# Performance work log

Hardware: AMD Instinct MI355X
Metric: run time of the kernel (lower is better)

The kernel has to match this reference:

```python
import jax, jax.numpy as jnp
import numpy as np

D_MODEL = 1024
NUM_HEADS = 16
D_LATENT = 256
HEAD_DIM = D_MODEL // NUM_HEADS
BATCH = 2048
SEQ = 32


def setup_inputs() -> dict:
    key = jax.random.key(0)
    ks = jax.random.split(key, 9)
    s = 1.0 / np.sqrt(D_MODEL)
    sl = 1.0 / np.sqrt(D_LATENT)
    return {
        "x": jax.random.normal(ks[0], (BATCH, SEQ, D_MODEL), dtype=jnp.float32),
        "memory": jax.random.normal(ks[1], (BATCH, SEQ, D_LATENT), dtype=jnp.float32),
        "W_q": jax.random.normal(ks[2], (D_MODEL, D_MODEL), dtype=jnp.float32) * s,
        "W_k": jax.random.normal(ks[3], (D_MODEL, D_MODEL), dtype=jnp.float32) * s,
        "W_v": jax.random.normal(ks[4], (D_MODEL, D_MODEL), dtype=jnp.float32) * s,
        "W_o": jax.random.normal(ks[5], (D_MODEL, D_MODEL), dtype=jnp.float32) * s,
        "W_down_kv": jax.random.normal(ks[6], (D_MODEL, D_LATENT), dtype=jnp.float32) * s,
        "W_up_k": jax.random.normal(ks[7], (D_LATENT, D_MODEL), dtype=jnp.float32) * sl,
        "W_up_v": jax.random.normal(ks[8], (D_LATENT, D_MODEL), dtype=jnp.float32) * sl,
    }


def reference(x, memory, W_q, W_k, W_v, W_o, W_down_kv, W_up_k, W_up_v):
    B, S, _ = x.shape
    q = x @ W_q                     # [B,S,D]
    k = x @ W_k
    v = x @ W_v
    latent_kv = (k + v) @ W_down_kv  # [B,S,L]
    latent_kv = jnp.nan_to_num((latent_kv + memory) * 0.5)
    k_rec = latent_kv @ W_up_k       # [B,S,D]
    v_rec = latent_kv @ W_up_v
    # split heads: [B,H,S,hd]
    qh = q.reshape(B, S, NUM_HEADS, HEAD_DIM).transpose(0, 2, 1, 3)
    kh = k_rec.reshape(B, S, NUM_HEADS, HEAD_DIM).transpose(0, 2, 1, 3)
    vh = v_rec.reshape(B, S, NUM_HEADS, HEAD_DIM).transpose(0, 2, 1, 3)
    # NOTE: faithful to source — scale is sqrt(d_model), not sqrt(head_dim)
    scores = jnp.einsum("bhqd,bhkd->bhqk", qh, kh) / jnp.sqrt(jnp.float32(D_MODEL))
    scores = jnp.nan_to_num(scores, nan=0.0, posinf=10.0, neginf=-10.0)
    attn = jax.nn.softmax(scores, axis=-1)
    ctx = jnp.einsum("bhqk,bhkd->bhqd", attn, vh)
    ctx = ctx.transpose(0, 2, 1, 3).reshape(B, S, D_MODEL)
    out = ctx @ W_o
    return out, latent_kv
```

## Files before the change

kernel.cpp:

```cpp
#include <hip/hip_runtime.h>
#include <hip/hip_bf16.h>

typedef unsigned short u16;
typedef __attribute__((ext_vector_type(8))) __bf16 bf16x8;
typedef __attribute__((ext_vector_type(8))) unsigned short u16x8;
typedef __attribute__((ext_vector_type(4))) float floatx4;
typedef __attribute__((ext_vector_type(16))) float floatx16;

#define AS1 __attribute__((address_space(1)))
#define AS3 __attribute__((address_space(3)))

__device__ __forceinline__ u16 f2bf(float f) {
  unsigned u = __float_as_uint(f);
  u += 0x7fffu + ((u >> 16) & 1u);
  return (u16)(u >> 16);
}

__device__ __forceinline__ void g2lds16(const u16* g, u16* l) {
  __builtin_amdgcn_global_load_lds((AS1 void*)g, (AS3 void*)l, 16, 0, 0);
}

__global__ __launch_bounds__(256) void k_cvt_bf16(const float* __restrict__ s,
                                                  u16* __restrict__ d, long n) {
  long i = ((long)blockIdx.x * blockDim.x + threadIdx.x) * 8;
  long stride = (long)gridDim.x * blockDim.x * 8;
  for (; i < n; i += stride) {
    float4 a = *(const float4*)(s + i);
    float4 b = *(const float4*)(s + i + 4);
    u16x8 o;
    o[0] = f2bf(a.x); o[1] = f2bf(a.y); o[2] = f2bf(a.z); o[3] = f2bf(a.w);
    o[4] = f2bf(b.x); o[5] = f2bf(b.y); o[6] = f2bf(b.z); o[7] = f2bf(b.w);
    *(u16x8*)(d + i) = o;
  }
}

__global__ __launch_bounds__(256) void k_addcvt(const float* __restrict__ s0,
                                                const float* __restrict__ s1,
                                                u16* __restrict__ d, long n) {
  long i = ((long)blockIdx.x * blockDim.x + threadIdx.x) * 8;
  long stride = (long)gridDim.x * blockDim.x * 8;
  for (; i < n; i += stride) {
    float4 a0 = *(const float4*)(s0 + i);
    float4 a1 = *(const float4*)(s0 + i + 4);
    float4 b0 = *(const float4*)(s1 + i);
    float4 b1 = *(const float4*)(s1 + i + 4);
    u16x8 o;
    o[0] = f2bf(a0.x + b0.x); o[1] = f2bf(a0.y + b0.y);
    o[2] = f2bf(a0.z + b0.z); o[3] = f2bf(a0.w + b0.w);
    o[4] = f2bf(a1.x + b1.x); o[5] = f2bf(a1.y + b1.y);
    o[6] = f2bf(a1.z + b1.z); o[7] = f2bf(a1.w + b1.w);
    *(u16x8*)(d + i) = o;
  }
}

__global__ __launch_bounds__(256) void k_tcvt(const float* __restrict__ s,
                                              u16* __restrict__ d, int R, int C) {
  __shared__ float t[32][33];
  const int lx = threadIdx.x, ly = threadIdx.y;
  const int bx = blockIdx.x * 32;
  const int by = blockIdx.y * 32;
  #pragma unroll
  for (int i = 0; i < 32; i += 8)
    t[ly + i][lx] = s[(size_t)(by + ly + i) * C + bx + lx];
  __syncthreads();
  #pragma unroll
  for (int i = 0; i < 32; i += 8)
    d[(size_t)(bx + ly + i) * R + by + lx] = f2bf(t[lx][ly + i]);
}


#define MFMA16(a, b, c) c = __builtin_amdgcn_mfma_f32_16x16x32_bf16(a, b, c, 0, 0, 0)

template <int MODE>
__global__ __launch_bounds__(256, 3) void gemm128(
    const u16* __restrict__ A, const u16* __restrict__ Bt,
    int M, int N, int K, int ntn,
    u16* __restrict__ Cb, float* __restrict__ Cf,
    const float* __restrict__ memp, float* __restrict__ latf, u16* __restrict__ latb) {
  __shared__ u16 As[128 * 64];
  __shared__ u16 Bs[128 * 64];
  const int tid = threadIdx.x;
  const int lane = tid & 63;
  const int wid = tid >> 6;
  const int wr = wid >> 1, wc = wid & 1;

  int bid = blockIdx.x;
  {
    const int nwg = gridDim.x;
    const int q = nwg >> 3, r = nwg & 7;
    const int xcd = bid & 7, idx = bid >> 3;
    bid = (xcd < r ? xcd * (q + 1) : r * (q + 1) + (xcd - r) * q) + idx;
  }
  const int mt = bid / ntn, nt = bid % ntn;
  const int m0 = mt * 128, n0 = nt * 128;

  const int fr = lane & 15;
  const int g8 = (lane >> 4) * 8;
  const int xr = (lane & 7) * 8;

  floatx4 acc[4][4];
  #pragma unroll
  for (int i = 0; i < 4; i++)
    #pragma unroll
    for (int j = 0; j < 4; j++) acc[i][j] = 0.0f;

  const u16* Ag0 = A + (size_t)m0 * K;
  const u16* Bg0 = Bt + (size_t)n0 * K;

  for (int kt = 0; kt < K; kt += 64) {
    #pragma unroll
    for (int p = 0; p < 4; p++) {
      int ci = p * 256 + tid;
      int row = ci >> 3;
      int kc = ((ci & 7) ^ (row & 7)) * 8;
      g2lds16(Ag0 + (size_t)row * K + kt + kc, &As[ci * 8]);
    }
    #pragma unroll
    for (int p = 0; p < 4; p++) {
      int ci = p * 256 + tid;
      int row = ci >> 3;
      int kc = ((ci & 7) ^ (row & 7)) * 8;
      g2lds16(Bg0 + (size_t)row * K + kt + kc, &Bs[ci * 8]);
    }
    __syncthreads();
    #pragma unroll
    for (int kk = 0; kk < 64; kk += 32) {
      const int koff = kk + g8;
      bf16x8 af[4], bfv[4];
      #pragma unroll
      for (int i = 0; i < 4; i++)
        af[i] = *(const bf16x8*)&As[(wr * 64 + i * 16 + fr) * 64 + (koff ^ xr)];
      #pragma unroll
      for (int j = 0; j < 4; j++)
        bfv[j] = *(const bf16x8*)&Bs[(wc * 64 + j * 16 + fr) * 64 + (koff ^ xr)];
      #pragma unroll
      for (int i = 0; i < 4; i++)
        #pragma unroll
        for (int j = 0; j < 4; j++)
          MFMA16(af[i], bfv[j], acc[i][j]);
    }
    __syncthreads();
  }

  #pragma unroll
  for (int i = 0; i < 4; i++) {
    const int mb = m0 + wr * 64 + i * 16 + ((lane >> 4) * 4);
    #pragma unroll
    for (int j = 0; j < 4; j++) {
      const int cb = n0 + wc * 64 + j * 16 + (lane & 15);
      #pragma unroll
      for (int r = 0; r < 4; r++) {
        const int m = mb + r;
        const float v = acc[i][j][r];
        if (MODE == 0) {
          Cb[(size_t)m * N + cb] = f2bf(v);
        } else if (MODE == 1) {
          if (n0 < 1024) {
            Cb[(size_t)m * 1024 + cb] = f2bf(v);
          } else {
            int lc = cb - 1024;
            float lv = (v + memp[(size_t)m * 256 + lc]) * 0.5f;
            latf[(size_t)m * 256 + lc] = lv;
            latb[(size_t)m * 256 + lc] = f2bf(lv);
          }
        } else {
          Cf[(size_t)m * N + cb] = v;
        }
      }
    }
  }
}

__global__ __launch_bounds__(256) void k_attn(const u16* __restrict__ KV, u16* Q) {
  __shared__ u16 Qs[4][32][72];
  __shared__ u16 Ks[4][32][72];
  __shared__ u16 Vt[4][64][40];
  const int tid = threadIdx.x;
  const int hg = blockIdx.x;
  const int b = blockIdx.y;
  const long tok0 = (long)b * 32;

  {
    const int t = tid >> 3, ci = tid & 7;
    const int hd = ci >> 1, c0 = (ci & 1) * 32;
    const u16* qrow = Q + (tok0 + t) * 1024 + hg * 256 + ci * 32;
    #pragma unroll
    for (int u = 0; u < 4; u++)
      *(u16x8*)&Qs[hd][t][c0 + u * 8] = *(const u16x8*)(qrow + u * 8);
    const u16* krow = KV + (tok0 + t) * 2048 + hg * 256 + ci * 32;
    #pragma unroll
    for (int u = 0; u < 4; u++)
      *(u16x8*)&Ks[hd][t][c0 + u * 8] = *(const u16x8*)(krow + u * 8);
    const u16* vrow = KV + (tok0 + t) * 2048 + 1024 + hg * 256 + ci * 32;
    #pragma unroll
    for (int u = 0; u < 4; u++) {
      u16x8 v = *(const u16x8*)(vrow + u * 8);
      #pragma unroll
      for (int j = 0; j < 8; j++) Vt[hd][c0 + u * 8 + j][t] = v[j];
    }
  }
  __syncthreads();

  const int w = tid >> 6;
  const int lane = tid & 63;
  const int col = lane & 31, hi = lane >> 5;

  floatx16 S;
  #pragma unroll
  for (int r = 0; r < 16; r++) S[r] = 0.0f;
  #pragma unroll
  for (int kc = 0; kc < 4; kc++) {
    bf16x8 aq = *(const bf16x8*)&Qs[w][col][kc * 16 + hi * 8];
    bf16x8 bk = *(const bf16x8*)&Ks[w][col][kc * 16 + hi * 8];
    S = __builtin_amdgcn_mfma_f32_32x32x16_bf16(aq, bk, S, 0, 0, 0);
  }

  u16* Pw = &Qs[w][0][0];
  float pr[16];
  #pragma unroll
  for (int r = 0; r < 16; r++) {
    float sc = S[r] * 0.03125f;
    float mx = sc;
    #pragma unroll
    for (int off = 16; off >= 1; off >>= 1) mx = fmaxf(mx, __shfl_xor(mx, off, 64));
    float e = __expf(sc - mx);
    float sm = e;
    #pragma unroll
    for (int off = 16; off >= 1; off >>= 1) sm += __shfl_xor(sm, off, 64);
    pr[r] = e / sm;
  }
  #pragma unroll
  for (int r = 0; r < 16; r++) {
    int row = (r & 3) + 8 * (r >> 2) + 4 * hi;
    Pw[row * 40 + col] = f2bf(pr[r]);
  }
  __syncthreads();

  floatx16 c0v, c1v;
  #pragma unroll
  for (int r = 0; r < 16; r++) { c0v[r] = 0.0f; c1v[r] = 0.0f; }
  #pragma unroll
  for (int kc = 0; kc < 2; kc++) {
    bf16x8 ap = *(const bf16x8*)&Pw[col * 40 + kc * 16 + hi * 8];
    bf16x8 bv0 = *(const bf16x8*)&Vt[w][col][kc * 16 + hi * 8];
    bf16x8 bv1 = *(const bf16x8*)&Vt[w][32 + col][kc * 16 + hi * 8];
    c0v = __builtin_amdgcn_mfma_f32_32x32x16_bf16(ap, bv0, c0v, 0, 0, 0);
    c1v = __builtin_amdgcn_mfma_f32_32x32x16_bf16(ap, bv1, c1v, 0, 0, 0);
  }
  #pragma unroll
  for (int r = 0; r < 16; r++) {
    int row = (r & 3) + 8 * (r >> 2) + 4 * hi;
    u16* orow = Q + (tok0 + row) * 1024 + hg * 256 + w * 64;
    orow[col] = f2bf(c0v[r]);
    orow[col + 32] = f2bf(c1v[r]);
  }
}

extern "C" void kernel_launch(void* const* d_in, const int* in_sizes, int n_in,
                              void* d_out, int out_size, void* d_ws, size_t ws_size,
                              hipStream_t stream) {
  const float* x    = (const float*)d_in[0];
  const float* mem  = (const float*)d_in[1];
  const float* W_q  = (const float*)d_in[2];
  const float* W_k  = (const float*)d_in[3];
  const float* W_v  = (const float*)d_in[4];
  const float* W_o  = (const float*)d_in[5];
  const float* W_dn = (const float*)d_in[6];
  const float* W_uk = (const float*)d_in[7];
  const float* W_uv = (const float*)d_in[8];
  float* out  = (float*)d_out;
  float* latf = out + (size_t)67108864;

  char* wp = (char*)d_ws;
  u16* Qb  = (u16*)wp; wp += (size_t)65536 * 1024 * 2;
  u16* Lb  = (u16*)wp; wp += (size_t)65536 * 256 * 2;
  u16* WAt = (u16*)wp; wp += (size_t)1280 * 1024 * 2;
  u16* WBt = (u16*)wp; wp += (size_t)2048 * 256 * 2;
  u16* Wot = (u16*)wp; wp += (size_t)1024 * 1024 * 2;
  u16* Wdt = (u16*)wp; wp += (size_t)256 * 1024 * 2;
  u16* Wkv = (u16*)wp; wp += (size_t)1024 * 1024 * 2;

  u16* Xb  = (u16*)d_out;
  u16* KVb = (u16*)d_out;

  dim3 b256(256);
  dim3 tb(32, 8);
  k_cvt_bf16<<<4096, b256, 0, stream>>>(x, Xb, (long)67108864);
  k_addcvt<<<512, b256, 0, stream>>>(W_k, W_v, Wkv, (long)1048576);
  k_tcvt<<<dim3(32, 32), tb, 0, stream>>>(W_q, WAt, 1024, 1024);
  k_tcvt<<<dim3(8, 32),  tb, 0, stream>>>(W_dn, Wdt, 1024, 256);
  k_tcvt<<<dim3(32, 8),  tb, 0, stream>>>(W_uk, WBt, 256, 1024);
  k_tcvt<<<dim3(32, 8),  tb, 0, stream>>>(W_uv, WBt + (size_t)1024 * 256, 256, 1024);
  k_tcvt<<<dim3(32, 32), tb, 0, stream>>>(W_o, Wot, 1024, 1024);

  gemm128<0><<<16, b256, 0, stream>>>(
      Wdt, Wkv, 256, 1024, 1024, 8, WAt + (size_t)1024 * 1024,
      nullptr, nullptr, nullptr, nullptr);

  gemm128<1><<<5120, b256, 0, stream>>>(
      Xb, WAt, 65536, 1280, 1024, 10, Qb, nullptr, mem, latf, Lb);

  gemm128<0><<<8192, b256, 0, stream>>>(
      Lb, WBt, 65536, 2048, 256, 16, KVb, nullptr, nullptr, nullptr, nullptr);

  k_attn<<<dim3(4, 2048), b256, 0, stream>>>(KVb, Qb);

  gemm128<2><<<4096, b256, 0, stream>>>(
      Qb, Wot, 65536, 1024, 1024, 8, nullptr, out, nullptr, nullptr, nullptr);
}
```

Before: 798.5 us.

## Fuse latent up-projection into attention via absorbed K/V weights

```diff
diff --git a/kernel.cpp b/kernel.cpp
--- a/kernel.cpp
+++ b/kernel.cpp
@@ -2,6 +2,7 @@
 #include <hip/hip_bf16.h>
 
 typedef unsigned short u16;
+typedef unsigned int u32;
 typedef __attribute__((ext_vector_type(8))) __bf16 bf16x8;
 typedef __attribute__((ext_vector_type(8))) unsigned short u16x8;
 typedef __attribute__((ext_vector_type(4))) float floatx4;
@@ -68,8 +69,8 @@
     d[(size_t)(bx + ly + i) * R + by + lx] = f2bf(t[lx][ly + i]);
 }
 
-
 #define MFMA16(a, b, c) c = __builtin_amdgcn_mfma_f32_16x16x32_bf16(a, b, c, 0, 0, 0)
+#define MFMA32(a, b, c) c = __builtin_amdgcn_mfma_f32_32x32x16_bf16(a, b, c, 0, 0, 0)
 
 template <int MODE>
 __global__ __launch_bounds__(256, 3) void gemm128(
@@ -171,88 +172,132 @@
   }
 }
 
-__global__ __launch_bounds__(256) void k_attn(const u16* __restrict__ KV, u16* Q) {
-  __shared__ u16 Qs[4][32][72];
-  __shared__ u16 Ks[4][32][72];
-  __shared__ u16 Vt[4][64][40];
+__device__ __forceinline__ void pack_lds(u16* T, const floatx16& d,
+                                         int col, int hi, bf16x8& f0, bf16x8& f1) {
+  #pragma unroll
+  for (int i = 0; i < 8; i++) {
+    const int r = 2 * i;
+    const int rr = (r & 3) + 8 * (r >> 2) + 4 * hi;
+    const u32 wv = (u32)f2bf(d[r]) | ((u32)f2bf(d[r + 1]) << 16);
+    *(u32*)&T[col * 40 + rr] = wv;
+  }
+  f0 = *(const bf16x8*)&T[col * 40 + hi * 8];
+  f1 = *(const bf16x8*)&T[col * 40 + 16 + hi * 8];
+}
+
+__global__ __launch_bounds__(256, 3) void k_attn2(
+    const u16* __restrict__ Lb,
+    u16* __restrict__ Q,
+    const u16* __restrict__ Wuk,
+    const u16* __restrict__ WuvT)
+{
+  __shared__ u16 Ls[32][264];
+  __shared__ u16 LsT[256][40];
+  __shared__ u16 Tw[4][32][40];
   const int tid = threadIdx.x;
-  const int hg = blockIdx.x;
-  const int b = blockIdx.y;
-  const long tok0 = (long)b * 32;
+  const long tok0 = (long)blockIdx.x * 32;
 
   {
-    const int t = tid >> 3, ci = tid & 7;
-    const int hd = ci >> 1, c0 = (ci & 1) * 32;
-    const u16* qrow = Q + (tok0 + t) * 1024 + hg * 256 + ci * 32;
-    #pragma unroll
-    for (int u = 0; u < 4; u++)
-      *(u16x8*)&Qs[hd][t][c0 + u * 8] = *(const u16x8*)(qrow + u * 8);
-    const u16* krow = KV + (tok0 + t) * 2048 + hg * 256 + ci * 32;
-    #pragma unroll
-    for (int u = 0; u < 4; u++)
-      *(u16x8*)&Ks[hd][t][c0 + u * 8] = *(const u16x8*)(krow + u * 8);
-    const u16* vrow = KV + (tok0 + t) * 2048 + 1024 + hg * 256 + ci * 32;
+    const int key = tid >> 3, c0 = (tid & 7) * 32;
     #pragma unroll
     for (int u = 0; u < 4; u++) {
-      u16x8 v = *(const u16x8*)(vrow + u * 8);
-      #pragma unroll
-      for (int j = 0; j < 8; j++) Vt[hd][c0 + u * 8 + j][t] = v[j];
+      u16x8 v = *(const u16x8*)(Lb + (tok0 + key) * 256 + c0 + u * 8);
+      *(u16x8*)&Ls[key][c0 + u * 8] = v;
+      #pragma unroll
+      for (int j = 0; j < 8; j++) LsT[c0 + u * 8 + j][key] = v[j];
     }
   }
   __syncthreads();
 
   const int w = tid >> 6;
   const int lane = tid & 63;
-  const int col = lane & 31, hi = lane >> 5;
-
-  floatx16 S;
-  #pragma unroll
-  for (int r = 0; r < 16; r++) S[r] = 0.0f;
-  #pragma unroll
-  for (int kc = 0; kc < 4; kc++) {
-    bf16x8 aq = *(const bf16x8*)&Qs[w][col][kc * 16 + hi * 8];
-    bf16x8 bk = *(const bf16x8*)&Ks[w][col][kc * 16 + hi * 8];
-    S = __builtin_amdgcn_mfma_f32_32x32x16_bf16(aq, bk, S, 0, 0, 0);
-  }
-
-  u16* Pw = &Qs[w][0][0];
-  float pr[16];
-  #pragma unroll
-  for (int r = 0; r < 16; r++) {
-    float sc = S[r] * 0.03125f;
-    float mx = sc;
-    #pragma unroll
-    for (int off = 16; off >= 1; off >>= 1) mx = fmaxf(mx, __shfl_xor(mx, off, 64));
-    float e = __expf(sc - mx);
-    float sm = e;
-    #pragma unroll
-    for (int off = 16; off >= 1; off >>= 1) sm += __shfl_xor(sm, off, 64);
-    pr[r] = e / sm;
-  }
-  #pragma unroll
-  for (int r = 0; r < 16; r++) {
-    int row = (r & 3) + 8 * (r >> 2) + 4 * hi;
-    Pw[row * 40 + col] = f2bf(pr[r]);
-  }
-  __syncthreads();
-
-  floatx16 c0v, c1v;
-  #pragma unroll
-  for (int r = 0; r < 16; r++) { c0v[r] = 0.0f; c1v[r] = 0.0f; }
-  #pragma unroll
-  for (int kc = 0; kc < 2; kc++) {
-    bf16x8 ap = *(const bf16x8*)&Pw[col * 40 + kc * 16 + hi * 8];
-    bf16x8 bv0 = *(const bf16x8*)&Vt[w][col][kc * 16 + hi * 8];
-    bf16x8 bv1 = *(const bf16x8*)&Vt[w][32 + col][kc * 16 + hi * 8];
-    c0v = __builtin_amdgcn_mfma_f32_32x32x16_bf16(ap, bv0, c0v, 0, 0, 0);
-    c1v = __builtin_amdgcn_mfma_f32_32x32x16_bf16(ap, bv1, c1v, 0, 0, 0);
-  }
-  #pragma unroll
-  for (int r = 0; r < 16; r++) {
-    int row = (r & 3) + 8 * (r >> 2) + 4 * hi;
-    u16* orow = Q + (tok0 + row) * 1024 + hg * 256 + w * 64;
-    orow[col] = f2bf(c0v[r]);
-    orow[col + 32] = f2bf(c1v[r]);
+  const int col = lane & 31;
+  const int hi = lane >> 5;
+  const int hi8 = hi * 8;
+  const int rhi4 = hi * 4;
+  u16* T = &Tw[w][0][0];
+
+  #pragma unroll 1
+  for (int hh = 0; hh < 4; hh++) {
+    const int h = w + hh * 4;
+
+    const u16* qbase = Q + (tok0 + col) * 1024 + h * 64 + hi8;
+    bf16x8 qf[4];
+    #pragma unroll
+    for (int ks = 0; ks < 4; ks++)
+      qf[ks] = *(const bf16x8*)(qbase + ks * 16);
+
+    floatx16 St;
+    #pragma unroll
+    for (int r = 0; r < 16; r++) St[r] = 0.0f;
+    #pragma unroll
+    for (int mi = 0; mi < 8; mi++) {
+      floatx16 qt;
+      #pragma unroll
+      for (int r = 0; r < 16; r++) qt[r] = 0.0f;
+      #pragma unroll
+      for (int ks = 0; ks < 4; ks++) {
+        bf16x8 af = *(const bf16x8*)(Wuk + (size_t)(mi * 32 + col) * 1024 +
+                                     h * 64 + ks * 16 + hi8);
+        MFMA32(af, qf[ks], qt);
+      }
+      bf16x8 qg0, qg1;
+      pack_lds(T, qt, col, hi, qg0, qg1);
+      bf16x8 la0 = *(const bf16x8*)&Ls[col][mi * 32 + hi8];
+      MFMA32(la0, qg0, St);
+      bf16x8 la1 = *(const bf16x8*)&Ls[col][mi * 32 + 16 + hi8];
+      MFMA32(la1, qg1, St);
+    }
+
+    float p[16];
+    float mx = -3.4e38f;
+    #pragma unroll
+    for (int r = 0; r < 16; r++) { p[r] = St[r] * 0.03125f; mx = fmaxf(mx, p[r]); }
+    mx = fmaxf(mx, __shfl_xor(mx, 32, 64));
+    float sm = 0.0f;
+    #pragma unroll
+    for (int r = 0; r < 16; r++) { p[r] = __expf(p[r] - mx); sm += p[r]; }
+    sm += __shfl_xor(sm, 32, 64);
+    const float rs = 1.0f / sm;
+    floatx16 Pt;
+    #pragma unroll
+    for (int r = 0; r < 16; r++) Pt[r] = p[r] * rs;
+    bf16x8 pg0, pg1;
+    pack_lds(T, Pt, col, hi, pg0, pg1);
+
+    floatx16 cacc0, cacc1;
+    #pragma unroll
+    for (int r = 0; r < 16; r++) { cacc0[r] = 0.0f; cacc1[r] = 0.0f; }
+    const u16* wv0 = WuvT + (size_t)(h * 64 + col) * 256;
+    const u16* wv1 = WuvT + (size_t)(h * 64 + 32 + col) * 256;
+    #pragma unroll
+    for (int mi = 0; mi < 8; mi++) {
+      floatx16 ct;
+      #pragma unroll
+      for (int r = 0; r < 16; r++) ct[r] = 0.0f;
+      bf16x8 lt0 = *(const bf16x8*)&LsT[mi * 32 + col][hi8];
+      MFMA32(lt0, pg0, ct);
+      bf16x8 lt1 = *(const bf16x8*)&LsT[mi * 32 + col][16 + hi8];
+      MFMA32(lt1, pg1, ct);
+      bf16x8 cg0, cg1;
+      pack_lds(T, ct, col, hi, cg0, cg1);
+      #pragma unroll
+      for (int ksl = 0; ksl < 2; ksl++) {
+        bf16x8 cg = ksl ? cg1 : cg0;
+        bf16x8 b0 = *(const bf16x8*)(wv0 + mi * 32 + ksl * 16 + hi8);
+        bf16x8 b1 = *(const bf16x8*)(wv1 + mi * 32 + ksl * 16 + hi8);
+        MFMA32(cg, b0, cacc0);
+        MFMA32(cg, b1, cacc1);
+      }
+    }
+
+    #pragma unroll
+    for (int r = 0; r < 16; r++) {
+      const int rr = (r & 3) + 8 * (r >> 2) + rhi4;
+      u16* orow = Q + (tok0 + rr) * 1024 + h * 64;
+      orow[col] = f2bf(cacc0[r]);
+      orow[32 + col] = f2bf(cacc1[r]);
+    }
   }
 }
 
@@ -272,25 +317,25 @@
   float* latf = out + (size_t)67108864;
 
   char* wp = (char*)d_ws;
-  u16* Qb  = (u16*)wp; wp += (size_t)65536 * 1024 * 2;
-  u16* Lb  = (u16*)wp; wp += (size_t)65536 * 256 * 2;
-  u16* WAt = (u16*)wp; wp += (size_t)1280 * 1024 * 2;
-  u16* WBt = (u16*)wp; wp += (size_t)2048 * 256 * 2;
-  u16* Wot = (u16*)wp; wp += (size_t)1024 * 1024 * 2;
-  u16* Wdt = (u16*)wp; wp += (size_t)256 * 1024 * 2;
-  u16* Wkv = (u16*)wp; wp += (size_t)1024 * 1024 * 2;
-
-  u16* Xb  = (u16*)d_out;
-  u16* KVb = (u16*)d_out;
+  u16* Qb   = (u16*)wp; wp += (size_t)65536 * 1024 * 2;
+  u16* Lb   = (u16*)wp; wp += (size_t)65536 * 256 * 2;
+  u16* WAt  = (u16*)wp; wp += (size_t)1280 * 1024 * 2;
+  u16* WuvT = (u16*)wp; wp += (size_t)1024 * 256 * 2;
+  u16* Wot  = (u16*)wp; wp += (size_t)1024 * 1024 * 2;
+  u16* Wdt  = (u16*)wp; wp += (size_t)256 * 1024 * 2;
+  u16* Wkv  = (u16*)wp; wp += (size_t)1024 * 1024 * 2;
+  u16* Wukb = (u16*)wp; wp += (size_t)256 * 1024 * 2;
+
+  u16* Xb = (u16*)d_out;
 
   dim3 b256(256);
   dim3 tb(32, 8);
   k_cvt_bf16<<<4096, b256, 0, stream>>>(x, Xb, (long)67108864);
   k_addcvt<<<512, b256, 0, stream>>>(W_k, W_v, Wkv, (long)1048576);
+  k_cvt_bf16<<<128, b256, 0, stream>>>(W_uk, Wukb, (long)262144);
   k_tcvt<<<dim3(32, 32), tb, 0, stream>>>(W_q, WAt, 1024, 1024);
   k_tcvt<<<dim3(8, 32),  tb, 0, stream>>>(W_dn, Wdt, 1024, 256);
-  k_tcvt<<<dim3(32, 8),  tb, 0, stream>>>(W_uk, WBt, 256, 1024);
-  k_tcvt<<<dim3(32, 8),  tb, 0, stream>>>(W_uv, WBt + (size_t)1024 * 256, 256, 1024);
+  k_tcvt<<<dim3(32, 8),  tb, 0, stream>>>(W_uv, WuvT, 256, 1024);
   k_tcvt<<<dim3(32, 32), tb, 0, stream>>>(W_o, Wot, 1024, 1024);
 
   gemm128<0><<<16, b256, 0, stream>>>(
@@ -300,10 +345,7 @@
   gemm128<1><<<5120, b256, 0, stream>>>(
       Xb, WAt, 65536, 1280, 1024, 10, Qb, nullptr, mem, latf, Lb);
 
-  gemm128<0><<<8192, b256, 0, stream>>>(
-      Lb, WBt, 65536, 2048, 256, 16, KVb, nullptr, nullptr, nullptr, nullptr);
-
-  k_attn<<<dim3(4, 2048), b256, 0, stream>>>(KVb, Qb);
+  k_attn2<<<2048, b256, 0, stream>>>(Lb, Qb, Wukb, WuvT);
 
   gemm128<2><<<4096, b256, 0, stream>>>(
       Qb, Wot, 65536, 1024, 1024, 8, nullptr, out, nullptr, nullptr, nullptr);
```

After: 898.1 us. 12.5% more time.

## Merge prep kernels into one launch and enlarge GEMM tiles to 256x128

Applied to the files above, without the earlier changes.

```diff
diff --git a/kernel.cpp b/kernel.cpp
--- a/kernel.cpp
+++ b/kernel.cpp
@@ -2,6 +2,7 @@
 #include <hip/hip_bf16.h>
 
 typedef unsigned short u16;
+typedef unsigned int u32;
 typedef __attribute__((ext_vector_type(8))) __bf16 bf16x8;
 typedef __attribute__((ext_vector_type(8))) unsigned short u16x8;
 typedef __attribute__((ext_vector_type(4))) float floatx4;
@@ -20,64 +21,82 @@
   __builtin_amdgcn_global_load_lds((AS1 void*)g, (AS3 void*)l, 16, 0, 0);
 }
 
-__global__ __launch_bounds__(256) void k_cvt_bf16(const float* __restrict__ s,
-                                                  u16* __restrict__ d, long n) {
-  long i = ((long)blockIdx.x * blockDim.x + threadIdx.x) * 8;
-  long stride = (long)gridDim.x * blockDim.x * 8;
-  for (; i < n; i += stride) {
-    float4 a = *(const float4*)(s + i);
-    float4 b = *(const float4*)(s + i + 4);
-    u16x8 o;
-    o[0] = f2bf(a.x); o[1] = f2bf(a.y); o[2] = f2bf(a.z); o[3] = f2bf(a.w);
-    o[4] = f2bf(b.x); o[5] = f2bf(b.y); o[6] = f2bf(b.z); o[7] = f2bf(b.w);
-    *(u16x8*)(d + i) = o;
-  }
-}
-
-__global__ __launch_bounds__(256) void k_addcvt(const float* __restrict__ s0,
-                                                const float* __restrict__ s1,
-                                                u16* __restrict__ d, long n) {
-  long i = ((long)blockIdx.x * blockDim.x + threadIdx.x) * 8;
-  long stride = (long)gridDim.x * blockDim.x * 8;
-  for (; i < n; i += stride) {
-    float4 a0 = *(const float4*)(s0 + i);
-    float4 a1 = *(const float4*)(s0 + i + 4);
-    float4 b0 = *(const float4*)(s1 + i);
-    float4 b1 = *(const float4*)(s1 + i + 4);
+__device__ __forceinline__ void tcvt_body(const float* __restrict__ s,
+                                          u16* __restrict__ d, int R, int C,
+                                          int bx, int by, int tid,
+                                          float (*t)[33]) {
+  const int lx = tid & 31, ly = tid >> 5;
+  const int x0 = bx * 32, y0 = by * 32;
+  #pragma unroll
+  for (int i = 0; i < 32; i += 8)
+    t[ly + i][lx] = s[(size_t)(y0 + ly + i) * C + x0 + lx];
+  __syncthreads();
+  #pragma unroll
+  for (int i = 0; i < 32; i += 8)
+    d[(size_t)(x0 + ly + i) * R + y0 + lx] = f2bf(t[lx][ly + i]);
+}
+
+__global__ __launch_bounds__(256) void k_prep(
+    const float* __restrict__ x, u16* __restrict__ Xb,
+    const float* __restrict__ Wk, const float* __restrict__ Wv, u16* __restrict__ Wkv,
+    const float* __restrict__ Wq, u16* __restrict__ WAt,
+    const float* __restrict__ Wdn, u16* __restrict__ Wdt,
+    const float* __restrict__ Wuk, u16* __restrict__ WBt,
+    const float* __restrict__ Wuv, u16* __restrict__ WBt2,
+    const float* __restrict__ Wo, u16* __restrict__ Wot) {
+  __shared__ float t[32][33];
+  const int b = blockIdx.x;
+  const int tid = threadIdx.x;
+  if (b < 4096) {
+    long i = ((long)b * 256 + tid) * 8;
+    const long stride = (long)4096 * 256 * 8;
+    for (; i < 67108864L; i += stride) {
+      float4 a = *(const float4*)(x + i);
+      float4 c = *(const float4*)(x + i + 4);
+      u16x8 o;
+      o[0] = f2bf(a.x); o[1] = f2bf(a.y); o[2] = f2bf(a.z); o[3] = f2bf(a.w);
+      o[4] = f2bf(c.x); o[5] = f2bf(c.y); o[6] = f2bf(c.z); o[7] = f2bf(c.w);
+      *(u16x8*)(Xb + i) = o;
+    }
+  } else if (b < 4608) {
+    long i = ((long)(b - 4096) * 256 + tid) * 8;
+    float4 a0 = *(const float4*)(Wk + i);
+    float4 a1 = *(const float4*)(Wk + i + 4);
+    float4 b0 = *(const float4*)(Wv + i);
+    float4 b1 = *(const float4*)(Wv + i + 4);
     u16x8 o;
     o[0] = f2bf(a0.x + b0.x); o[1] = f2bf(a0.y + b0.y);
     o[2] = f2bf(a0.z + b0.z); o[3] = f2bf(a0.w + b0.w);
     o[4] = f2bf(a1.x + b1.x); o[5] = f2bf(a1.y + b1.y);
     o[6] = f2bf(a1.z + b1.z); o[7] = f2bf(a1.w + b1.w);
-    *(u16x8*)(d + i) = o;
-  }
-}
-
-__global__ __launch_bounds__(256) void k_tcvt(const float* __restrict__ s,
-                                              u16* __restrict__ d, int R, int C) {
-  __shared__ float t[32][33];
-  const int lx = threadIdx.x, ly = threadIdx.y;
-  const int bx = blockIdx.x * 32;
-  const int by = blockIdx.y * 32;
-  #pragma unroll
-  for (int i = 0; i < 32; i += 8)
-    t[ly + i][lx] = s[(size_t)(by + ly + i) * C + bx + lx];
-  __syncthreads();
-  #pragma unroll
-  for (int i = 0; i < 32; i += 8)
-    d[(size_t)(bx + ly + i) * R + by + lx] = f2bf(t[lx][ly + i]);
-}
-
+    *(u16x8*)(Wkv + i) = o;
+  } else if (b < 5632) {
+    int lb = b - 4608;
+    tcvt_body(Wq, WAt, 1024, 1024, lb & 31, lb >> 5, tid, t);
+  } else if (b < 5888) {
+    int lb = b - 5632;
+    tcvt_body(Wdn, Wdt, 1024, 256, lb & 7, lb >> 3, tid, t);
+  } else if (b < 6144) {
+    int lb = b - 5888;
+    tcvt_body(Wuk, WBt, 256, 1024, lb & 31, lb >> 5, tid, t);
+  } else if (b < 6400) {
+    int lb = b - 6144;
+    tcvt_body(Wuv, WBt2, 256, 1024, lb & 31, lb >> 5, tid, t);
+  } else {
+    int lb = b - 6400;
+    tcvt_body(Wo, Wot, 1024, 1024, lb & 31, lb >> 5, tid, t);
+  }
+}
 
 #define MFMA16(a, b, c) c = __builtin_amdgcn_mfma_f32_16x16x32_bf16(a, b, c, 0, 0, 0)
 
 template <int MODE>
-__global__ __launch_bounds__(256, 3) void gemm128(
+__global__ __launch_bounds__(512, 4) void gemm_mn(
     const u16* __restrict__ A, const u16* __restrict__ Bt,
     int M, int N, int K, int ntn,
     u16* __restrict__ Cb, float* __restrict__ Cf,
     const float* __restrict__ memp, float* __restrict__ latf, u16* __restrict__ latb) {
-  __shared__ u16 As[128 * 64];
+  __shared__ u16 As[256 * 64];
   __shared__ u16 Bs[128 * 64];
   const int tid = threadIdx.x;
   const int lane = tid & 63;
@@ -92,7 +111,7 @@
     bid = (xcd < r ? xcd * (q + 1) : r * (q + 1) + (xcd - r) * q) + idx;
   }
   const int mt = bid / ntn, nt = bid % ntn;
-  const int m0 = mt * 128, n0 = nt * 128;
+  const int m0 = mt * 256, n0 = nt * 128;
 
   const int fr = lane & 15;
   const int g8 = (lane >> 4) * 8;
@@ -110,14 +129,14 @@
   for (int kt = 0; kt < K; kt += 64) {
     #pragma unroll
     for (int p = 0; p < 4; p++) {
-      int ci = p * 256 + tid;
+      int ci = p * 512 + tid;
       int row = ci >> 3;
       int kc = ((ci & 7) ^ (row & 7)) * 8;
       g2lds16(Ag0 + (size_t)row * K + kt + kc, &As[ci * 8]);
     }
     #pragma unroll
-    for (int p = 0; p < 4; p++) {
-      int ci = p * 256 + tid;
+    for (int p = 0; p < 2; p++) {
+      int ci = p * 512 + tid;
       int row = ci >> 3;
       int kc = ((ci & 7) ^ (row & 7)) * 8;
       g2lds16(Bg0 + (size_t)row * K + kt + kc, &Bs[ci * 8]);
@@ -284,27 +303,24 @@
   u16* KVb = (u16*)d_out;
 
   dim3 b256(256);
-  dim3 tb(32, 8);
-  k_cvt_bf16<<<4096, b256, 0, stream>>>(x, Xb, (long)67108864);
-  k_addcvt<<<512, b256, 0, stream>>>(W_k, W_v, Wkv, (long)1048576);
-  k_tcvt<<<dim3(32, 32), tb, 0, stream>>>(W_q, WAt, 1024, 1024);
-  k_tcvt<<<dim3(8, 32),  tb, 0, stream>>>(W_dn, Wdt, 1024, 256);
-  k_tcvt<<<dim3(32, 8),  tb, 0, stream>>>(W_uk, WBt, 256, 1024);
-  k_tcvt<<<dim3(32, 8),  tb, 0, stream>>>(W_uv, WBt + (size_t)1024 * 256, 256, 1024);
-  k_tcvt<<<dim3(32, 32), tb, 0, stream>>>(W_o, Wot, 1024, 1024);
-
-  gemm128<0><<<16, b256, 0, stream>>>(
+  dim3 b512(512);
+
+  k_prep<<<7424, b256, 0, stream>>>(
+      x, Xb, W_k, W_v, Wkv, W_q, WAt, W_dn, Wdt,
+      W_uk, WBt, W_uv, WBt + (size_t)1024 * 256, W_o, Wot);
+
+  gemm_mn<0><<<8, b512, 0, stream>>>(
       Wdt, Wkv, 256, 1024, 1024, 8, WAt + (size_t)1024 * 1024,
       nullptr, nullptr, nullptr, nullptr);
 
-  gemm128<1><<<5120, b256, 0, stream>>>(
+  gemm_mn<1><<<2560, b512, 0, stream>>>(
       Xb, WAt, 65536, 1280, 1024, 10, Qb, nullptr, mem, latf, Lb);
 
-  gemm128<0><<<8192, b256, 0, stream>>>(
+  gemm_mn<0><<<4096, b512, 0, stream>>>(
       Lb, WBt, 65536, 2048, 256, 16, KVb, nullptr, nullptr, nullptr, nullptr);
 
   k_attn<<<dim3(4, 2048), b256, 0, stream>>>(KVb, Qb);
 
-  gemm128<2><<<4096, b256, 0, stream>>>(
+  gemm_mn<2><<<2048, b512, 0, stream>>>(
       Qb, Wot, 65536, 1024, 1024, 8, nullptr, out, nullptr, nullptr, nullptr);
 }
```

After: 841.3 us. 1.05x slower.
